# Optimization experiments

Measured on AMD Instinct MI355X. Metric: run time of the kernel, lower is better.

## Reference

```python
import jax, jax.numpy as jnp
import numpy as np

DIM = 1024
HEADS = 16
DIM_HEAD = 64
INNER = HEADS * DIM_HEAD  # 1024
SCALE = DIM_HEAD ** -0.5


def layernorm(x, gamma, beta, eps=1e-5):
    mu = jnp.mean(x, axis=-1, keepdims=True)
    var = jnp.var(x, axis=-1, keepdims=True)
    return (x - mu) * jax.lax.rsqrt(var + eps) * gamma + beta


def setup_inputs() -> dict:
    key = jax.random.key(0)
    ks = jax.random.split(key, 6)
    x = jax.random.normal(ks[0], (2, 2048, DIM), dtype=jnp.float32)
    # params (stored [in, out]; torch Linear does x @ W.T with W [out, in])
    w_q = jax.random.normal(ks[1], (DIM, INNER), dtype=jnp.float32) * (DIM ** -0.5)
    w_kv = jax.random.normal(ks[2], (DIM, 2 * INNER), dtype=jnp.float32) * (DIM ** -0.5)
    w_out = jax.random.normal(ks[3], (INNER, DIM), dtype=jnp.float32) * (INNER ** -0.5)
    b_out = jnp.zeros((DIM,), dtype=jnp.float32)
    gamma = jnp.ones((DIM,), dtype=jnp.float32)
    beta = jnp.zeros((DIM,), dtype=jnp.float32)
    return {"x": x, "w_q": w_q, "w_kv": w_kv, "w_out": w_out, "b_out": b_out,
            "gamma": gamma, "beta": beta}


def reference(x, w_q, w_kv, w_out, b_out, gamma, beta):
    b, n, _ = x.shape
    xn = layernorm(x, gamma, beta)
    q = xn @ w_q                           # [b, n, inner]
    kv = xn @ w_kv                         # [b, n, 2*inner]
    k, v = jnp.split(kv, 2, axis=-1)
    def split_heads(t):
        return t.reshape(b, n, HEADS, DIM_HEAD).transpose(0, 2, 1, 3)  # b h n d
    q, k, v = split_heads(q), split_heads(k), split_heads(v)
    dots = jnp.einsum('bhid,bhjd->bhij', q, k) * SCALE   # [b, h, n, n]
    attn = jax.nn.softmax(dots, axis=-1)
    out = jnp.einsum('bhij,bhjd->bhid', attn, v)          # [b, h, n, d]
    out = out.transpose(0, 2, 1, 3).reshape(b, n, INNER)  # b n (h d)
    return out @ w_out + b_out
```

## Files before the change

kernel.cpp:

```cpp
#include <hip/hip_runtime.h>

typedef unsigned short u16;
typedef u16   u16x8 __attribute__((ext_vector_type(8)));
typedef __bf16 bf16x8 __attribute__((ext_vector_type(8)));
typedef float f32x4 __attribute__((ext_vector_type(4)));
typedef float f32x2 __attribute__((ext_vector_type(2)));
typedef _Float16 f16x4 __attribute__((ext_vector_type(4)));
typedef _Float16 f16x8 __attribute__((ext_vector_type(8)));
typedef unsigned u32x2 __attribute__((ext_vector_type(2)));

__device__ __forceinline__ u16 f2b(float f){ __bf16 h=(__bf16)f; return __builtin_bit_cast(u16,h); }

__device__ __forceinline__ float ex2(float x){
#if __has_builtin(__builtin_amdgcn_exp2f)
  return __builtin_amdgcn_exp2f(x);
#else
  float r; asm("v_exp_f32 %0, %1" : "=v"(r) : "v"(x)); return r;
#endif
}

__device__ __forceinline__ f32x4 mfma16(u16x8 a, u16x8 b, f32x4 c){
  return __builtin_amdgcn_mfma_f32_16x16x32_bf16(
      __builtin_bit_cast(bf16x8,a), __builtin_bit_cast(bf16x8,b), c, 0,0,0);
}

__device__ __forceinline__ void gl2lds16(const u16* g, u16* l){
  __builtin_amdgcn_global_load_lds((const __attribute__((address_space(1))) void*)g,
                                   (__attribute__((address_space(3))) void*)l, 16, 0, 0);
}

__global__ __launch_bounds__(256) void ln_kernel(const float* __restrict__ x,
                                                 const float* __restrict__ gamma,
                                                 const float* __restrict__ beta,
                                                 u16* __restrict__ xn){
  const int row = blockIdx.x, t = threadIdx.x;
  const float4 v = ((const float4*)(x + (size_t)row*1024))[t];
  float s  = v.x+v.y+v.z+v.w;
  float sq = v.x*v.x+v.y*v.y+v.z*v.z+v.w*v.w;
  for (int m=1;m<64;m<<=1){ s += __shfl_xor(s,m); sq += __shfl_xor(sq,m); }
  __shared__ float red[8];
  const int w=t>>6, l=t&63;
  if(l==0){ red[w]=s; red[4+w]=sq; }
  __syncthreads();
  const float S  = red[0]+red[1]+red[2]+red[3];
  const float SQ = red[4]+red[5]+red[6]+red[7];
  const float mu = S*(1.f/1024.f);
  const float var= SQ*(1.f/1024.f)-mu*mu;
  const float rs = rsqrtf(var+1e-5f);
  const float4 g4=((const float4*)gamma)[t], b4=((const float4*)beta)[t];
  u16 o0=f2b((v.x-mu)*rs*g4.x+b4.x);
  u16 o1=f2b((v.y-mu)*rs*g4.y+b4.y);
  u16 o2=f2b((v.z-mu)*rs*g4.z+b4.z);
  u16 o3=f2b((v.w-mu)*rs*g4.w+b4.w);
  uint2 p; p.x=(unsigned)o0|((unsigned)o1<<16); p.y=(unsigned)o2|((unsigned)o3<<16);
  ((uint2*)(xn + (size_t)row*1024))[t]=p;
}

__global__ __launch_bounds__(256) void wtrans_all_kernel(const float* __restrict__ wq,
    const float* __restrict__ wkv, const float* __restrict__ wout,
    u16* __restrict__ wqkvt, u16* __restrict__ woutt){
  __shared__ float tile[64][65];
  const int bx=blockIdx.x, t=threadIdx.x;
  const float* in; u16* out; int C, cxx;
  if(bx<16){ in=wq;  out=wqkvt;           C=1024; cxx=bx; }
  else if(bx<48){ in=wkv; out=wqkvt+1024*1024; C=2048; cxx=bx-16; }
  else { in=wout; out=woutt;             C=1024; cxx=bx-48; }
  const int R=1024;
  const int c0=cxx*64, r0=blockIdx.y*64;
  {
    const int r=t>>2, cc=t&3;
    const float* gp = in + (size_t)(r0+r)*C + c0 + cc*16;
    #pragma unroll
    for(int i=0;i<4;i++){
      float4 f=((const float4*)gp)[i];
      tile[r][cc*16+i*4+0]=f.x; tile[r][cc*16+i*4+1]=f.y;
      tile[r][cc*16+i*4+2]=f.z; tile[r][cc*16+i*4+3]=f.w;
    }
  }
  __syncthreads();
  const int c=t>>2, rc=t&3;
  u16x8 a,b;
  #pragma unroll
  for(int i=0;i<8;i++) a[i]=f2b(tile[rc*16+i][c]);
  #pragma unroll
  for(int i=0;i<8;i++) b[i]=f2b(tile[rc*16+8+i][c]);
  u16* op = out + (size_t)(c0+c)*R + r0 + rc*16;
  *(u16x8*)op=a; *(u16x8*)(op+8)=b;
}

template<int MODE,int TM>
__global__ __launch_bounds__(256) void gemm_bt_kernel(const u16* __restrict__ A,
    const u16* __restrict__ Bt, u16* __restrict__ outQ, u16* __restrict__ outK,
    u16* __restrict__ outV, float* __restrict__ outF, const float* __restrict__ bias,
    float scale, int M, int N, int K){
  constexpr int MT = TM/32;
  __shared__ u16 As[TM*64];
  __shared__ u16 Bs[128*64];
  const int t=threadIdx.x, w=t>>6, l=t&63, qd=l>>4, ln=l&15;
  const int m0=blockIdx.y*TM, n0=blockIdx.x*128;
  const int wm=(w>>1)*(TM/2), wn=(w&1)*64;
  f32x4 acc[MT][4] = {};
  const int nK = K>>6;
  for(int kt=0; kt<nK; kt++){
    const int k0=kt*64;
    #pragma unroll
    for(int p=0;p<MT;p++){
      const int cid=p*256+t, r=cid>>3, pc=cid&7, g=pc^(r&7);
      gl2lds16(A + (size_t)(m0+r)*K + k0 + g*8, &As[(p*256 + (t&192))*8]);
    }
    #pragma unroll
    for(int p=0;p<4;p++){
      const int cid=p*256+t, r=cid>>3, pc=cid&7, g=pc^(r&7);
      gl2lds16(Bt + (size_t)(n0+r)*K + k0 + g*8, &Bs[(p*256 + (t&192))*8]);
    }
    __syncthreads();
    #pragma unroll
    for(int ks=0;ks<2;ks++){
      u16x8 af[MT], bf[4];
      #pragma unroll
      for(int mt=0;mt<MT;mt++){
        const int m=wm+mt*16+ln, kc=ks*4+qd, pcc=kc^(m&7);
        af[mt]=*(const u16x8*)&As[m*64 + pcc*8];
      }
      #pragma unroll
      for(int nt=0;nt<4;nt++){
        const int n=wn+nt*16+ln, kc=ks*4+qd, pcc=kc^(n&7);
        bf[nt]=*(const u16x8*)&Bs[n*64 + pcc*8];
      }
      #pragma unroll
      for(int mt=0;mt<MT;mt++)
        #pragma unroll
        for(int nt=0;nt<4;nt++)
          acc[mt][nt]=mfma16(af[mt],bf[nt],acc[mt][nt]);
    }
    __syncthreads();
  }
  if(MODE==1){
    #pragma unroll
    for(int mt=0;mt<MT;mt++)
      #pragma unroll
      for(int rr=0;rr<4;rr++){
        const int row = m0+wm+mt*16+qd*4+rr;
        #pragma unroll
        for(int nt=0;nt<4;nt++){
          const int col = n0+wn+nt*16+ln;
          outF[(size_t)row*N+col]=acc[mt][nt][rr]+bias[col];
        }
      }
  } else if(n0<1024){
    #pragma unroll
    for(int mt=0;mt<MT;mt++)
      #pragma unroll
      for(int rr=0;rr<4;rr++){
        const int row = m0+wm+mt*16+qd*4+rr;
        #pragma unroll
        for(int nt=0;nt<4;nt++)
          outQ[(size_t)row*1024 + n0+wn+nt*16+ln]=f2b(acc[mt][nt][rr]*scale);
      }
  } else if(n0<2048){
    u16* kp = outK + (size_t)((m0>>11)*16 + ((n0-1024+wn)>>6))*131072;
    const int jb = (m0&2047) + wm;
    #pragma unroll
    for(int mt=0;mt<MT;mt++)
      #pragma unroll
      for(int rr=0;rr<4;rr++){
        const int j = jb + mt*16 + qd*4 + rr;
        #pragma unroll
        for(int nt=0;nt<4;nt++)
          kp[(size_t)j*64 + nt*16+ln]=f2b(acc[mt][nt][rr]);
      }
  } else {
    u16* vpp = outV + (size_t)((m0>>11)*16 + ((n0-2048+wn)>>6))*131072;
    const int jb = (m0&2047) + wm;
    #pragma unroll
    for(int mt=0;mt<MT;mt++){
      const int j = jb + mt*16 + qd*4;
      const int vbase = ((j>>5)*4 + ((j>>2)&3))*512 + ((j>>4)&1)*4;
      #pragma unroll
      for(int nt=0;nt<4;nt++){
        const auto lo=__builtin_amdgcn_cvt_pkrtz(acc[mt][nt][0],acc[mt][nt][1]);
        const auto hi=__builtin_amdgcn_cvt_pkrtz(acc[mt][nt][2],acc[mt][nt][3]);
        uint2 w2; w2.x=__builtin_bit_cast(unsigned,lo); w2.y=__builtin_bit_cast(unsigned,hi);
        *(uint2*)&vpp[vbase + (nt*16+ln)*8] = w2;
      }
    }
  }
}

__global__ __launch_bounds__(512,4) void attn_kernel(const u16* __restrict__ Q,
    const u16* __restrict__ Kp, const u16* __restrict__ Vp, u16* __restrict__ O){
  __shared__ u16 Ks[2][8192];
  __shared__ u16 Vs[2][8192];
  const int qt=blockIdx.x, h=blockIdx.y, bb=blockIdx.z;
  const int t=threadIdx.x, w=t>>6, l=t&63, qd=l>>4, ln=l&15;
  const int q0=qt*128;
  const size_t baseQ=(size_t)bb*2048*1024 + h*64;
  const size_t baseKV=(size_t)(bb*16+h)*131072;
  u16x8 qf[2];
  #pragma unroll
  for(int ks=0;ks<2;ks++)
    qf[ks] = *(const u16x8*)(Q + baseQ + (size_t)(q0+w*16+ln)*1024 + ks*32+qd*8);
  f32x4 o_acc[4]={};
  f32x4 l_acc={};
  const f16x4 onesB={(_Float16)1.f,(_Float16)1.f,(_Float16)1.f,(_Float16)1.f};
  const f32x4 zf={0.f,0.f,0.f,0.f};

  auto stage=[&](int buf,int j0){
    #pragma unroll
    for(int p=0;p<2;p++){
      const int cid=p*512+t, r=cid>>3, g=(t&7)^((t>>3)&7);
      gl2lds16(Kp + baseKV + (size_t)(j0+r)*64 + g*8, &Ks[buf][(p*512+(t&448))*8]);
    }
    #pragma unroll
    for(int p=0;p<2;p++)
      gl2lds16(Vp + baseKV + (size_t)(j0>>5)*2048 + (size_t)(p*512+t)*8,
               &Vs[buf][(p*512+(t&448))*8]);
  };

  stage(0,0);
  __syncthreads();
  int cur=0;
  for(int jt=0;jt<16;jt++){
    if(jt<15) stage(cur^1,(jt+1)*128);
    const u16* Kb=&Ks[cur][0];
    const u16* Vb=&Vs[cur][0];
    #pragma unroll
    for(int jh=0;jh<2;jh++){
      f16x8 vall[2][4];
      #pragma unroll
      for(int al=0;al<2;al++)
        #pragma unroll
        for(int dt=0;dt<4;dt++)
          vall[al][dt]=*(const f16x8*)&Vb[(((jh*2+al)*4+qd)*64 + dt*16+ln)*8];
      f32x4 s[4];
      #pragma unroll
      for(int ks=0;ks<2;ks++){
        u16x8 kf[4];
        #pragma unroll
        for(int j4=0;j4<4;j4++){
          const int row=(jh*4+j4)*16+ln;
          kf[j4]=*(const u16x8*)&Kb[row*64 + (((ks*4+qd)^(ln&7))*8)];
        }
        __builtin_amdgcn_s_setprio(1);
        #pragma unroll
        for(int j4=0;j4<4;j4++)
          s[j4] = ks? mfma16(kf[j4],qf[1],s[j4]) : mfma16(kf[j4],qf[0],zf);
        __builtin_amdgcn_s_setprio(0);
      }
      #pragma unroll
      for(int al=0;al<2;al++){
        #pragma unroll
        for(int tt=0;tt<2;tt++){
          const int j4l=al*2+tt;
          const float p0=ex2(s[j4l][0]), p1=ex2(s[j4l][1]);
          const float p2=ex2(s[j4l][2]), p3=ex2(s[j4l][3]);
          const auto lo=__builtin_amdgcn_cvt_pkrtz(p0,p1);
          const auto hi=__builtin_amdgcn_cvt_pkrtz(p2,p3);
          u32x2 pu; pu.x=__builtin_bit_cast(unsigned,lo); pu.y=__builtin_bit_cast(unsigned,hi);
          const f16x4 pf=__builtin_bit_cast(f16x4,pu);
          __builtin_amdgcn_s_setprio(1);
          l_acc=__builtin_amdgcn_mfma_f32_16x16x16f16(pf,onesB,l_acc,0,0,0);
          #pragma unroll
          for(int dt=0;dt<4;dt++){
            const f16x4 vf=tt? __builtin_shufflevector(vall[al][dt],vall[al][dt],4,5,6,7)
                             : __builtin_shufflevector(vall[al][dt],vall[al][dt],0,1,2,3);
            o_acc[dt]=__builtin_amdgcn_mfma_f32_16x16x16f16(pf,vf,o_acc[dt],0,0,0);
          }
          __builtin_amdgcn_s_setprio(0);
        }
      }
    }
    __syncthreads();
    cur^=1;
  }

  #pragma unroll
  for(int rr=0;rr<4;rr++){
    const float lr=1.f/l_acc[rr];
    const int row=q0+w*16+qd*4+rr;
    #pragma unroll
    for(int dt=0;dt<4;dt++)
      O[baseQ + (size_t)row*1024 + dt*16+ln]=f2b(o_acc[dt][rr]*lr);
  }
}

extern "C" void kernel_launch(void* const* d_in, const int* in_sizes, int n_in,
                              void* d_out, int out_size, void* d_ws, size_t ws_size,
                              hipStream_t stream) {
  const float* x     = (const float*)d_in[0];
  const float* w_q   = (const float*)d_in[1];
  const float* w_kv  = (const float*)d_in[2];
  const float* w_out = (const float*)d_in[3];
  const float* b_out = (const float*)d_in[4];
  const float* gamma = (const float*)d_in[5];
  const float* beta  = (const float*)d_in[6];
  float* out = (float*)d_out;

  char* ws=(char*)d_ws;
  size_t off=0;
  u16* xn    =(u16*)(ws+off); off += (size_t)4096*1024*2;
  u16* wqkvt =(u16*)(ws+off); off += (size_t)3072*1024*2;
  u16* woutt =(u16*)(ws+off); off += (size_t)1024*1024*2;
  u16* qb    =(u16*)(ws+off); off += (size_t)4096*1024*2;
  u16* kpb   =(u16*)(ws+off); off += (size_t)4096*1024*2;
  u16* vpb   =(u16*)(ws+off); off += (size_t)4096*1024*2;
  u16* ob    =(u16*)(ws+off); off += (size_t)4096*1024*2;

  ln_kernel<<<4096,256,0,stream>>>(x,gamma,beta,xn);
  wtrans_all_kernel<<<dim3(64,16),256,0,stream>>>(w_q,w_kv,w_out,wqkvt,woutt);

  const float SCALE_Q = 0.125f*1.4426950408889634f;
  gemm_bt_kernel<2,128><<<dim3(24,32),256,0,stream>>>(xn,wqkvt,qb,kpb,vpb,nullptr,nullptr,SCALE_Q,4096,3072,1024);
  attn_kernel<<<dim3(16,16,2),512,0,stream>>>(qb,kpb,vpb,ob);
  gemm_bt_kernel<1,64><<<dim3(8,64),256,0,stream>>>(ob,woutt,nullptr,nullptr,nullptr,out,b_out,1.f,4096,1024,1024);
}
```

Before: 188.9 us.

## Use 16x16x32 f16 MFMA for PV with permuted K/V layouts

```diff
diff --git a/kernel.cpp b/kernel.cpp
--- a/kernel.cpp
+++ b/kernel.cpp
@@ -8,6 +8,7 @@
 typedef _Float16 f16x4 __attribute__((ext_vector_type(4)));
 typedef _Float16 f16x8 __attribute__((ext_vector_type(8)));
 typedef unsigned u32x2 __attribute__((ext_vector_type(2)));
+typedef unsigned u32x4 __attribute__((ext_vector_type(4)));
 
 __device__ __forceinline__ u16 f2b(float f){ __bf16 h=(__bf16)f; return __builtin_bit_cast(u16,h); }
 
@@ -22,6 +23,10 @@
 __device__ __forceinline__ f32x4 mfma16(u16x8 a, u16x8 b, f32x4 c){
   return __builtin_amdgcn_mfma_f32_16x16x32_bf16(
       __builtin_bit_cast(bf16x8,a), __builtin_bit_cast(bf16x8,b), c, 0,0,0);
+}
+
+__device__ __forceinline__ f32x4 mfma32h(f16x8 a, f16x8 b, f32x4 c){
+  return __builtin_amdgcn_mfma_f32_16x16x32_f16(a, b, c, 0,0,0);
 }
 
 __device__ __forceinline__ void gl2lds16(const u16* g, u16* l){
@@ -175,13 +180,14 @@
     #pragma unroll
     for(int mt=0;mt<MT;mt++){
       const int j = jb + mt*16 + qd*4;
-      const int vbase = ((j>>5)*4 + ((j>>2)&3))*512 + ((j>>4)&1)*4;
+      const int grp = (j>>5)*4 + ((j>>3)&3);
+      const int sub = j&7;
       #pragma unroll
       for(int nt=0;nt<4;nt++){
         const auto lo=__builtin_amdgcn_cvt_pkrtz(acc[mt][nt][0],acc[mt][nt][1]);
         const auto hi=__builtin_amdgcn_cvt_pkrtz(acc[mt][nt][2],acc[mt][nt][3]);
         uint2 w2; w2.x=__builtin_bit_cast(unsigned,lo); w2.y=__builtin_bit_cast(unsigned,hi);
-        *(uint2*)&vpp[vbase + (nt*16+ln)*8] = w2;
+        *(uint2*)&vpp[(size_t)(grp*64 + nt*16+ln)*8 + sub] = w2;
       }
     }
   }
@@ -202,15 +208,22 @@
     qf[ks] = *(const u16x8*)(Q + baseQ + (size_t)(q0+w*16+ln)*1024 + ks*32+qd*8);
   f32x4 o_acc[4]={};
   f32x4 l_acc={};
-  const f16x4 onesB={(_Float16)1.f,(_Float16)1.f,(_Float16)1.f,(_Float16)1.f};
+  const f16x8 onesB={(_Float16)1.f,(_Float16)1.f,(_Float16)1.f,(_Float16)1.f,
+                     (_Float16)1.f,(_Float16)1.f,(_Float16)1.f,(_Float16)1.f};
   const f32x4 zf={0.f,0.f,0.f,0.f};
 
+  int koff[2];
+  #pragma unroll
+  for(int p=0;p<2;p++){
+    const int r=(p*512+t)>>3, g=(t&7)^(r&7);
+    const int pr=(r&~31)+((r>>2)&3)*8+((r>>4)&1)*4+(r&3);
+    koff[p]=pr*64+g*8;
+  }
+
   auto stage=[&](int buf,int j0){
     #pragma unroll
-    for(int p=0;p<2;p++){
-      const int cid=p*512+t, r=cid>>3, g=(t&7)^((t>>3)&7);
-      gl2lds16(Kp + baseKV + (size_t)(j0+r)*64 + g*8, &Ks[buf][(p*512+(t&448))*8]);
-    }
+    for(int p=0;p<2;p++)
+      gl2lds16(Kp + baseKV + (size_t)j0*64 + koff[p], &Ks[buf][(p*512+(t&448))*8]);
     #pragma unroll
     for(int p=0;p<2;p++)
       gl2lds16(Vp + baseKV + (size_t)(j0>>5)*2048 + (size_t)(p*512+t)*8,
@@ -249,25 +262,19 @@
       }
       #pragma unroll
       for(int al=0;al<2;al++){
-        #pragma unroll
-        for(int tt=0;tt<2;tt++){
-          const int j4l=al*2+tt;
-          const float p0=ex2(s[j4l][0]), p1=ex2(s[j4l][1]);
-          const float p2=ex2(s[j4l][2]), p3=ex2(s[j4l][3]);
-          const auto lo=__builtin_amdgcn_cvt_pkrtz(p0,p1);
-          const auto hi=__builtin_amdgcn_cvt_pkrtz(p2,p3);
-          u32x2 pu; pu.x=__builtin_bit_cast(unsigned,lo); pu.y=__builtin_bit_cast(unsigned,hi);
-          const f16x4 pf=__builtin_bit_cast(f16x4,pu);
-          __builtin_amdgcn_s_setprio(1);
-          l_acc=__builtin_amdgcn_mfma_f32_16x16x16f16(pf,onesB,l_acc,0,0,0);
-          #pragma unroll
-          for(int dt=0;dt<4;dt++){
-            const f16x4 vf=tt? __builtin_shufflevector(vall[al][dt],vall[al][dt],4,5,6,7)
-                             : __builtin_shufflevector(vall[al][dt],vall[al][dt],0,1,2,3);
-            o_acc[dt]=__builtin_amdgcn_mfma_f32_16x16x16f16(pf,vf,o_acc[dt],0,0,0);
-          }
-          __builtin_amdgcn_s_setprio(0);
-        }
+        const int t0=al*2, t1=al*2+1;
+        u32x4 pw;
+        pw.x=__builtin_bit_cast(unsigned,__builtin_amdgcn_cvt_pkrtz(ex2(s[t0][0]),ex2(s[t0][1])));
+        pw.y=__builtin_bit_cast(unsigned,__builtin_amdgcn_cvt_pkrtz(ex2(s[t0][2]),ex2(s[t0][3])));
+        pw.z=__builtin_bit_cast(unsigned,__builtin_amdgcn_cvt_pkrtz(ex2(s[t1][0]),ex2(s[t1][1])));
+        pw.w=__builtin_bit_cast(unsigned,__builtin_amdgcn_cvt_pkrtz(ex2(s[t1][2]),ex2(s[t1][3])));
+        const f16x8 pf=__builtin_bit_cast(f16x8,pw);
+        __builtin_amdgcn_s_setprio(1);
+        l_acc=mfma32h(pf,onesB,l_acc);
+        #pragma unroll
+        for(int dt=0;dt<4;dt++)
+          o_acc[dt]=mfma32h(pf,vall[al][dt],o_acc[dt]);
+        __builtin_amdgcn_s_setprio(0);
       }
     }
     __syncthreads();
@@ -312,5 +319,5 @@
   const float SCALE_Q = 0.125f*1.4426950408889634f;
   gemm_bt_kernel<2,128><<<dim3(24,32),256,0,stream>>>(xn,wqkvt,qb,kpb,vpb,nullptr,nullptr,SCALE_Q,4096,3072,1024);
   attn_kernel<<<dim3(16,16,2),512,0,stream>>>(qb,kpb,vpb,ob);
-  gemm_bt_kernel<1,64><<<dim3(8,64),256,0,stream>>>(ob,woutt,nullptr,nullptr,nullptr,out,b_out,1.f,4096,1024,1024);
-}
+  gemm_bt_kernel<1,128><<<dim3(8,32),256,0,stream>>>(ob,woutt,nullptr,nullptr,nullptr,out,b_out,1.f,4096,1024,1024);
+}
```

After: 195.9 us. 1.04x slower.
